# Kernel optimization log

Measured on AMD Instinct MI355X. Metric: run time of the kernel, lower is better.

## Reference

```python
import jax, jax.numpy as jnp
import numpy as np


def setup_inputs() -> dict:
    key = jax.random.key(0)
    ks = jax.random.split(key, 10)
    B, T, I, H = 64, 512, 512, 1024
    stdv = 1.0 / np.sqrt(H)
    u = lambda k, shape: jax.random.uniform(k, shape, jnp.float32, -stdv, stdv)
    return {
        "x": jax.random.normal(ks[0], (B, T, I), jnp.float32),
        "mask": jnp.ones((B, T, 1), jnp.float32),
        "s0": jnp.zeros((B, H), jnp.float32),
        "Ws": u(ks[1], (H, I)),
        "Wr": u(ks[2], (H, I)),
        "Wz": u(ks[3], (H, I)),
        "Us": u(ks[4], (H, H)),
        "Ur": u(ks[5], (H, H)),
        "Uz": u(ks[6], (H, H)),
        "bs": u(ks[7], (H,)),
        "br": u(ks[8], (H,)),
        "bz": u(ks[9], (H,)),
    }


def reference(x, mask, s0, Ws, Wr, Wz, Us, Ur, Uz, bs, br, bz):
    # Precompute input projections for all timesteps (batched GEMM).
    # x: [B,T,I]; xg: [B,T,H]
    xz = jnp.einsum("bti,hi->bth", x, Wz) + bz
    xr = jnp.einsum("bti,hi->bth", x, Wr) + br
    xs = jnp.einsum("bti,hi->bth", x, Ws) + bs

    def step(s, inp):
        xz_t, xr_t, xs_t, m_t = inp  # [B,H],[B,H],[B,H],[B,1]
        z = jax.nn.sigmoid(xz_t + s @ Uz.T)
        r = jax.nn.sigmoid(xr_t + s @ Ur.T)
        s_hat = jax.nn.relu(xs_t + (s * r) @ Us.T)
        s_new = (1.0 - z) * s + z * s_hat
        s_new = s * (1.0 - m_t) + s_new * m_t
        return s_new, s_new

    # scan over time: move T to leading axis
    xs_t = (jnp.swapaxes(xz, 0, 1), jnp.swapaxes(xr, 0, 1),
            jnp.swapaxes(xs, 0, 1), jnp.swapaxes(mask, 0, 1))
    _, ys = jax.lax.scan(step, s0, xs_t)  # ys: [T,B,H]
    return jnp.swapaxes(ys, 0, 1)  # [B,T,H]
```

## Files before the change

### kernel.cpp

```cpp
#include <hip/hip_runtime.h>

typedef unsigned short u16;
typedef unsigned long long u64;
typedef float f32x4 __attribute__((ext_vector_type(4)));
typedef short s16x8 __attribute__((ext_vector_type(8)));

#define B_ 64
#define T_ 512
#define I_ 512
#define H_ 1024
#define NBLK 256
#define NGRP 4
#define NMEM 64
#define NTHR 256

#define OFF_FLG 0
#define OFF_SBF 32768
#define OFF_RS  (OFF_SBF + 131072)
#define OFF_U   (OFF_RS + 131072)
#define OFF_W   (OFF_U + 6291456)

__device__ __forceinline__ u16 f2bf(float f) {
  unsigned u = __float_as_uint(f);
  return (u16)((u + 0x7FFFu + ((u >> 16) & 1u)) >> 16);
}

__device__ __forceinline__ s16x8 pack8(float4 a, float4 b) {
  s16x8 r;
  r[0] = (short)f2bf(a.x); r[1] = (short)f2bf(a.y);
  r[2] = (short)f2bf(a.z); r[3] = (short)f2bf(a.w);
  r[4] = (short)f2bf(b.x); r[5] = (short)f2bf(b.y);
  r[6] = (short)f2bf(b.z); r[7] = (short)f2bf(b.w);
  return r;
}

__device__ __forceinline__ void ld16_sc1(s16x8* d, const char* p) {
  asm volatile("global_load_dwordx4 %0, %1, off sc0 sc1" : "=v"(*d) : "v"(p));
}
__device__ __forceinline__ void st16_sc1(char* p, s16x8 v) {
  asm volatile("global_store_dwordx4 %0, %1, off sc0 sc1" :: "v"(p), "v"(v) : "memory");
}

__global__ void prep_kernel(const float* __restrict__ s0,
                            const float* __restrict__ Wz, const float* __restrict__ Wr,
                            const float* __restrict__ Ws, const float* __restrict__ Uz,
                            const float* __restrict__ Ur, const float* __restrict__ Us,
                            char* __restrict__ ws) {
  u16* ubf = (u16*)(ws + OFF_U);
  u16* wbf = (u16*)(ws + OFF_W);
  int tid = blockIdx.x * blockDim.x + threadIdx.x;
  int stride = gridDim.x * blockDim.x;
  const int NU = H_ * H_;
  for (int i = tid; i < NU; i += stride) {
    ubf[i] = f2bf(Uz[i]);
    ubf[NU + i] = f2bf(Ur[i]);
    ubf[2 * NU + i] = f2bf(Us[i]);
  }
  const int NW = H_ * I_;
  for (int i = tid; i < NW; i += stride) {
    wbf[i] = f2bf(Wz[i]);
    wbf[NW + i] = f2bf(Wr[i]);
    wbf[2 * NW + i] = f2bf(Ws[i]);
  }
  for (int f = tid; f < 4 * 32 * 64; f += stride) {
    int kc = (f >> 6) & 31, l = f & 63;
    int b = (f >> 11) * 16 + (l & 15);
    int k = kc * 32 + (l >> 4) * 8;
    const float* sp = s0 + (u64)b * H_ + k;
    ushort4 lo, hi;
    lo.x = f2bf(sp[0]); lo.y = f2bf(sp[1]); lo.z = f2bf(sp[2]); lo.w = f2bf(sp[3]);
    hi.x = f2bf(sp[4]); hi.y = f2bf(sp[5]); hi.z = f2bf(sp[6]); hi.w = f2bf(sp[7]);
    ushort4* dst = (ushort4*)(ws + OFF_SBF + (u64)f * 16);
    dst[0] = lo; dst[1] = hi;
  }
}

__device__ __forceinline__ void bar_poll(const unsigned* flags, int bg, unsigned bidx) {
  if (threadIdx.x < NMEM) {
    while (__hip_atomic_load(flags + (u64)(bg * NMEM + threadIdx.x) * 32,
                             __ATOMIC_RELAXED, __HIP_MEMORY_SCOPE_AGENT) < bidx)
      __builtin_amdgcn_s_sleep(1);
  }
  __syncthreads();
}

#define SWZ(row, byteInRow, rowShift) \
  (((((row) << (rowShift)) + (byteInRow))) ^ (((row) & 7) << 4))

__global__ __launch_bounds__(NTHR, 1) void scan_kernel(
    const float* __restrict__ x, const float* __restrict__ mask,
    const float* __restrict__ bz, const float* __restrict__ br,
    const float* __restrict__ bs, const float* __restrict__ s0,
    char* __restrict__ ws, float* __restrict__ out) {

  __shared__ u16 u_lds[3 * 16 * 1024];
  __shared__ u16 w_lds[3 * 16 * 512];
  __shared__ f32x4 red[4][2][64];
  __shared__ u16 tbf[16][16];
  __shared__ float tf32[16][16];

  char* fsb = ws + OFF_SBF;
  char* frb = ws + OFF_RS;
  const u16* ubf = (const u16*)(ws + OFF_U);
  const u16* wbf = (const u16*)(ws + OFF_W);
  unsigned* flags = (unsigned*)(ws + OFF_FLG);

  const int tid = threadIdx.x;
  const int jb = blockIdx.x;
  const int bg = jb & 3;
  const int hs = jb >> 2;
  const int h0 = hs * 16;
  const int lane = tid & 63;
  const int wave = tid >> 6;
  const int ln15 = lane & 15;
  const int kg = lane >> 4;
  const int h = h0 + ln15;

  for (int e = tid * 8; e < 3 * 16 * 1024; e += NTHR * 8) {
    int row = e >> 10, k = e & 1023;
    int g = row >> 4, hi = row & 15;
    uint4 v = *(const uint4*)(ubf + ((u64)(g * H_ + h0 + hi) * H_ + k));
    *(uint4*)((char*)u_lds + SWZ(row, (k << 1), 11)) = v;
  }
  for (int e = tid * 8; e < 3 * 16 * 512; e += NTHR * 8) {
    int row = e >> 9, k = e & 511;
    int g = row >> 4, hi = row & 15;
    uint4 v = *(const uint4*)(wbf + ((u64)(g * H_ + h0 + hi) * I_ + k));
    *(uint4*)((char*)w_lds + SWZ(row, (k << 1), 10)) = v;
  }
  const float bzv = bz[h];
  const float brv = br[h];
  const float bsv = bs[h];
  float sreg[4];
  #pragma unroll
  for (int j = 0; j < 4; ++j)
    sreg[j] = s0[(u64)(bg * 16 + kg * 4 + j) * H_ + h];
  __syncthreads();

  const char* sbase = fsb + (((u64)bg * 32 + wave * 8) * 64 + lane) * 16;
  const char* rbase = frb + (((u64)bg * 32 + wave * 8) * 64 + lane) * 16;
  char* sdst = fsb + (((u64)bg * 32 + (hs >> 1)) * 64 + lane + 32 * (hs & 1)) * 16;
  char* rdst = frb + (((u64)bg * 32 + (hs >> 1)) * 64 + lane + 32 * (hs & 1)) * 16;

  s16x8 xf[4];
  #pragma unroll
  for (int i = 0; i < 4; ++i) {
    const float* xp = x + ((u64)(bg * 16 + ln15) * T_) * I_ + (wave * 4 + i) * 32 + kg * 8;
    xf[i] = pack8(*(const float4*)xp, *(const float4*)(xp + 4));
  }
  f32x4 axz = {0.f,0.f,0.f,0.f}, axr = {0.f,0.f,0.f,0.f}, axs = {0.f,0.f,0.f,0.f};
  #pragma unroll
  for (int i = 0; i < 4; ++i) {
    const int cb = (wave * 4 + i) * 64 + kg * 16;
    s16x8 w0 = *(const s16x8*)((const char*)w_lds + SWZ(ln15, cb, 10));
    s16x8 w1 = *(const s16x8*)((const char*)w_lds + SWZ(16 + ln15, cb, 10));
    s16x8 w2 = *(const s16x8*)((const char*)w_lds + SWZ(32 + ln15, cb, 10));
    axz = __builtin_amdgcn_mfma_f32_16x16x32_bf16(xf[i], w0, axz, 0, 0, 0);
    axr = __builtin_amdgcn_mfma_f32_16x16x32_bf16(xf[i], w1, axr, 0, 0, 0);
    axs = __builtin_amdgcn_mfma_f32_16x16x32_bf16(xf[i], w2, axs, 0, 0, 0);
  }
  unsigned bidx = 0;

  for (int t = 0; t < T_; ++t) {
    float mv[4], zv[4];
    if (wave == 0) {
      #pragma unroll
      for (int j = 0; j < 4; ++j) mv[j] = mask[(u64)(bg * 16 + kg * 4 + j) * T_ + t];
    }

    s16x8 aS[8];
    #pragma unroll
    for (int q = 0; q < 8; ++q) ld16_sc1(&aS[q], sbase + q * 1024);
    __builtin_amdgcn_sched_barrier(0);
    asm volatile("s_waitcnt vmcnt(0)" ::: "memory");
    __builtin_amdgcn_sched_barrier(0);
    f32x4 accz = axz, accr = axr;
    #pragma unroll
    for (int q = 0; q < 8; ++q) {
      const int cb = (wave * 8 + q) * 64 + kg * 16;
      s16x8 b0 = *(const s16x8*)((const char*)u_lds + SWZ(ln15, cb, 11));
      s16x8 b1 = *(const s16x8*)((const char*)u_lds + SWZ(16 + ln15, cb, 11));
      accz = __builtin_amdgcn_mfma_f32_16x16x32_bf16(aS[q], b0, accz, 0, 0, 0);
      accr = __builtin_amdgcn_mfma_f32_16x16x32_bf16(aS[q], b1, accr, 0, 0, 0);
    }
    red[wave][0][lane] = accz;
    red[wave][1][lane] = accr;
    __syncthreads();
    ++bidx;
    if (wave == 0) {
      f32x4 az = red[0][0][lane], ar = red[0][1][lane];
      #pragma unroll
      for (int w = 1; w < 4; ++w) { az += red[w][0][lane]; ar += red[w][1][lane]; }
      #pragma unroll
      for (int j = 0; j < 4; ++j) {
        float z = 1.f / (1.f + __expf(-(az[j] + bzv)));
        float r = 1.f / (1.f + __expf(-(ar[j] + brv)));
        zv[j] = z;
        tbf[kg * 4 + j][ln15] = f2bf(sreg[j] * r);
      }
      if (lane < 32) {
        s16x8 v = *(const s16x8*)&tbf[lane & 15][(lane >> 4) * 8];
        st16_sc1(rdst, v);
      }
      asm volatile("s_waitcnt vmcnt(0)" ::: "memory");
      if (lane == 0)
        __hip_atomic_store(flags + (u64)(bg * NMEM + hs) * 32, bidx,
                           __ATOMIC_RELAXED, __HIP_MEMORY_SCOPE_AGENT);
    }
    bar_poll(flags, bg, bidx);

    s16x8 aR[8];
    #pragma unroll
    for (int q = 0; q < 8; ++q) ld16_sc1(&aR[q], rbase + q * 1024);
    __builtin_amdgcn_sched_barrier(0);
    asm volatile("s_waitcnt vmcnt(0)" ::: "memory");
    __builtin_amdgcn_sched_barrier(0);
    f32x4 accs = axs;
    #pragma unroll
    for (int q = 0; q < 8; ++q) {
      const int cb = (wave * 8 + q) * 64 + kg * 16;
      s16x8 b2 = *(const s16x8*)((const char*)u_lds + SWZ(32 + ln15, cb, 11));
      accs = __builtin_amdgcn_mfma_f32_16x16x32_bf16(aR[q], b2, accs, 0, 0, 0);
    }
    red[wave][0][lane] = accs;
    __syncthreads();
    ++bidx;
    if (wave == 0) {
      f32x4 as_ = red[0][0][lane];
      #pragma unroll
      for (int w = 1; w < 4; ++w) as_ += red[w][0][lane];
      #pragma unroll
      for (int j = 0; j < 4; ++j) {
        float shat = fmaxf(as_[j] + bsv, 0.f);
        float sn = (1.f - zv[j]) * sreg[j] + zv[j] * shat;
        float sf = sreg[j] + mv[j] * (sn - sreg[j]);
        sreg[j] = sf;
        tf32[kg * 4 + j][ln15] = sf;
        tbf[kg * 4 + j][ln15] = f2bf(sf);
      }
      if (lane < 32) {
        s16x8 v = *(const s16x8*)&tbf[lane & 15][(lane >> 4) * 8];
        st16_sc1(sdst, v);
      }
      asm volatile("s_waitcnt vmcnt(0)" ::: "memory");
      if (lane == 0)
        __hip_atomic_store(flags + (u64)(bg * NMEM + hs) * 32, bidx,
                           __ATOMIC_RELAXED, __HIP_MEMORY_SCOPE_AGENT);
      {
        f32x4 o = *(const f32x4*)&tf32[lane >> 2][(lane & 3) * 4];
        f32x4* op = (f32x4*)(out + ((u64)(bg * 16 + (lane >> 2)) * T_ + t) * H_ + h0 + (lane & 3) * 4);
        __builtin_nontemporal_store(o, op);
      }
    }
    if (t + 1 < T_) {
      #pragma unroll
      for (int i = 0; i < 4; ++i) {
        const float* xp = x + ((u64)(bg * 16 + ln15) * T_ + (t + 1)) * I_ + (wave * 4 + i) * 32 + kg * 8;
        xf[i] = pack8(*(const float4*)xp, *(const float4*)(xp + 4));
      }
      axz = f32x4{0.f,0.f,0.f,0.f}; axr = f32x4{0.f,0.f,0.f,0.f}; axs = f32x4{0.f,0.f,0.f,0.f};
      #pragma unroll
      for (int i = 0; i < 4; ++i) {
        const int cb = (wave * 4 + i) * 64 + kg * 16;
        s16x8 w0 = *(const s16x8*)((const char*)w_lds + SWZ(ln15, cb, 10));
        s16x8 w1 = *(const s16x8*)((const char*)w_lds + SWZ(16 + ln15, cb, 10));
        s16x8 w2 = *(const s16x8*)((const char*)w_lds + SWZ(32 + ln15, cb, 10));
        axz = __builtin_amdgcn_mfma_f32_16x16x32_bf16(xf[i], w0, axz, 0, 0, 0);
        axr = __builtin_amdgcn_mfma_f32_16x16x32_bf16(xf[i], w1, axr, 0, 0, 0);
        axs = __builtin_amdgcn_mfma_f32_16x16x32_bf16(xf[i], w2, axs, 0, 0, 0);
      }
    }
    bar_poll(flags, bg, bidx);
  }
}

extern "C" void kernel_launch(void* const* d_in, const int* in_sizes, int n_in,
                              void* d_out, int out_size, void* d_ws, size_t ws_size,
                              hipStream_t stream) {
  const float* x   = (const float*)d_in[0];
  const float* msk = (const float*)d_in[1];
  const float* s0  = (const float*)d_in[2];
  const float* Ws_ = (const float*)d_in[3];
  const float* Wr_ = (const float*)d_in[4];
  const float* Wz_ = (const float*)d_in[5];
  const float* Us_ = (const float*)d_in[6];
  const float* Ur_ = (const float*)d_in[7];
  const float* Uz_ = (const float*)d_in[8];
  const float* bs_ = (const float*)d_in[9];
  const float* br_ = (const float*)d_in[10];
  const float* bz_ = (const float*)d_in[11];
  float* out = (float*)d_out;
  char* ws = (char*)d_ws;

  (void)hipMemsetAsync(d_ws, 0, 32768, stream);
  hipLaunchKernelGGL(prep_kernel, dim3(1024), dim3(256), 0, stream,
                     s0, Wz_, Wr_, Ws_, Uz_, Ur_, Us_, ws);
  hipLaunchKernelGGL(scan_kernel, dim3(NBLK), dim3(NTHR), 0, stream,
                     x, msk, bz_, br_, bs_, s0, ws, out);
}
```

Baseline: 2.649 ms.

## Distribute gate epilogue across all waves with per-wave flags and polling

```diff
diff --git a/kernel.cpp b/kernel.cpp
--- a/kernel.cpp
+++ b/kernel.cpp
@@ -15,7 +15,7 @@
 #define NTHR 256
 
 #define OFF_FLG 0
-#define OFF_SBF 32768
+#define OFF_SBF 131072
 #define OFF_RS  (OFF_SBF + 131072)
 #define OFF_U   (OFF_RS + 131072)
 #define OFF_W   (OFF_U + 6291456)
@@ -75,15 +75,6 @@
   }
 }
 
-__device__ __forceinline__ void bar_poll(const unsigned* flags, int bg, unsigned bidx) {
-  if (threadIdx.x < NMEM) {
-    while (__hip_atomic_load(flags + (u64)(bg * NMEM + threadIdx.x) * 32,
-                             __ATOMIC_RELAXED, __HIP_MEMORY_SCOPE_AGENT) < bidx)
-      __builtin_amdgcn_s_sleep(1);
-  }
-  __syncthreads();
-}
-
 #define SWZ(row, byteInRow, rowShift) \
   (((((row) << (rowShift)) + (byteInRow))) ^ (((row) & 7) << 4))
 
@@ -95,9 +86,9 @@
 
   __shared__ u16 u_lds[3 * 16 * 1024];
   __shared__ u16 w_lds[3 * 16 * 512];
-  __shared__ f32x4 red[4][2][64];
-  __shared__ u16 tbf[16][16];
-  __shared__ float tf32[16][16];
+  __shared__ f32x4 red1[4][2][64];
+  __shared__ f32x4 red2[4][64];
+  __shared__ u16 tbw[4][4][16];
 
   char* fsb = ws + OFF_SBF;
   char* frb = ws + OFF_RS;
@@ -115,6 +106,7 @@
   const int ln15 = lane & 15;
   const int kg = lane >> 4;
   const int h = h0 + ln15;
+  const int Bl = 4 * wave + kg;
 
   for (int e = tid * 8; e < 3 * 16 * 1024; e += NTHR * 8) {
     int row = e >> 10, k = e & 1023;
@@ -131,16 +123,17 @@
   const float bzv = bz[h];
   const float brv = br[h];
   const float bsv = bs[h];
-  float sreg[4];
-  #pragma unroll
-  for (int j = 0; j < 4; ++j)
-    sreg[j] = s0[(u64)(bg * 16 + kg * 4 + j) * H_ + h];
+  float sreg = s0[(u64)(bg * 16 + Bl) * H_ + h];
+  float mv = mask[(u64)(bg * 16 + Bl) * T_];
   __syncthreads();
 
   const char* sbase = fsb + (((u64)bg * 32 + wave * 8) * 64 + lane) * 16;
   const char* rbase = frb + (((u64)bg * 32 + wave * 8) * 64 + lane) * 16;
-  char* sdst = fsb + (((u64)bg * 32 + (hs >> 1)) * 64 + lane + 32 * (hs & 1)) * 16;
-  char* rdst = frb + (((u64)bg * 32 + (hs >> 1)) * 64 + lane + 32 * (hs & 1)) * 16;
+  const int lp = (4 * wave + (lane & 3)) + 16 * ((hs & 1) * 2 + ((lane >> 2) & 1));
+  char* sdst = fsb + (((u64)bg * 32 + (hs >> 1)) * 64 + lp) * 16;
+  char* rdst = frb + (((u64)bg * 32 + (hs >> 1)) * 64 + lp) * 16;
+  unsigned* myflag = flags + ((u64)(bg * NMEM + hs) * 4 + wave) * 32;
+  const unsigned* pollp = flags + ((u64)(bg * NMEM + wave * 16 + ln15) * 4 + kg) * 32;
 
   s16x8 xf[4];
   #pragma unroll
@@ -160,14 +153,9 @@
     axs = __builtin_amdgcn_mfma_f32_16x16x32_bf16(xf[i], w2, axs, 0, 0, 0);
   }
   unsigned bidx = 0;
+  float zval = 0.f;
 
   for (int t = 0; t < T_; ++t) {
-    float mv[4], zv[4];
-    if (wave == 0) {
-      #pragma unroll
-      for (int j = 0; j < 4; ++j) mv[j] = mask[(u64)(bg * 16 + kg * 4 + j) * T_ + t];
-    }
-
     s16x8 aS[8];
     #pragma unroll
     for (int q = 0; q < 8; ++q) ld16_sc1(&aS[q], sbase + q * 1024);
@@ -183,31 +171,33 @@
       accz = __builtin_amdgcn_mfma_f32_16x16x32_bf16(aS[q], b0, accz, 0, 0, 0);
       accr = __builtin_amdgcn_mfma_f32_16x16x32_bf16(aS[q], b1, accr, 0, 0, 0);
     }
-    red[wave][0][lane] = accz;
-    red[wave][1][lane] = accr;
+    red1[wave][0][lane] = accz;
+    red1[wave][1][lane] = accr;
     __syncthreads();
     ++bidx;
-    if (wave == 0) {
-      f32x4 az = red[0][0][lane], ar = red[0][1][lane];
-      #pragma unroll
-      for (int w = 1; w < 4; ++w) { az += red[w][0][lane]; ar += red[w][1][lane]; }
-      #pragma unroll
-      for (int j = 0; j < 4; ++j) {
-        float z = 1.f / (1.f + __expf(-(az[j] + bzv)));
-        float r = 1.f / (1.f + __expf(-(ar[j] + brv)));
-        zv[j] = z;
-        tbf[kg * 4 + j][ln15] = f2bf(sreg[j] * r);
-      }
-      if (lane < 32) {
-        s16x8 v = *(const s16x8*)&tbf[lane & 15][(lane >> 4) * 8];
+    {
+      float az = 0.f, ar = 0.f;
+      #pragma unroll
+      for (int w2 = 0; w2 < 4; ++w2) {
+        const float* pz = (const float*)&red1[w2][0][wave * 16 + ln15];
+        const float* pr = (const float*)&red1[w2][1][wave * 16 + ln15];
+        az += pz[kg];
+        ar += pr[kg];
+      }
+      float z = 1.f / (1.f + __expf(-(az + bzv)));
+      float r = 1.f / (1.f + __expf(-(ar + brv)));
+      zval = z;
+      tbw[wave][kg][ln15] = f2bf(sreg * r);
+      if (lane < 8) {
+        s16x8 v = *(const s16x8*)&tbw[wave][lane & 3][((lane >> 2) & 1) * 8];
         st16_sc1(rdst, v);
       }
       asm volatile("s_waitcnt vmcnt(0)" ::: "memory");
       if (lane == 0)
-        __hip_atomic_store(flags + (u64)(bg * NMEM + hs) * 32, bidx,
-                           __ATOMIC_RELAXED, __HIP_MEMORY_SCOPE_AGENT);
-    }
-    bar_poll(flags, bg, bidx);
+        __hip_atomic_store(myflag, bidx, __ATOMIC_RELAXED, __HIP_MEMORY_SCOPE_AGENT);
+    }
+    while (__hip_atomic_load(pollp, __ATOMIC_RELAXED, __HIP_MEMORY_SCOPE_AGENT) < bidx)
+      __builtin_amdgcn_s_sleep(1);
 
     s16x8 aR[8];
     #pragma unroll
@@ -222,35 +212,29 @@
       s16x8 b2 = *(const s16x8*)((const char*)u_lds + SWZ(32 + ln15, cb, 11));
       accs = __builtin_amdgcn_mfma_f32_16x16x32_bf16(aR[q], b2, accs, 0, 0, 0);
     }
-    red[wave][0][lane] = accs;
+    red2[wave][lane] = accs;
     __syncthreads();
     ++bidx;
-    if (wave == 0) {
-      f32x4 as_ = red[0][0][lane];
-      #pragma unroll
-      for (int w = 1; w < 4; ++w) as_ += red[w][0][lane];
-      #pragma unroll
-      for (int j = 0; j < 4; ++j) {
-        float shat = fmaxf(as_[j] + bsv, 0.f);
-        float sn = (1.f - zv[j]) * sreg[j] + zv[j] * shat;
-        float sf = sreg[j] + mv[j] * (sn - sreg[j]);
-        sreg[j] = sf;
-        tf32[kg * 4 + j][ln15] = sf;
-        tbf[kg * 4 + j][ln15] = f2bf(sf);
-      }
-      if (lane < 32) {
-        s16x8 v = *(const s16x8*)&tbf[lane & 15][(lane >> 4) * 8];
+    {
+      float as_ = 0.f;
+      #pragma unroll
+      for (int w2 = 0; w2 < 4; ++w2) {
+        const float* ps = (const float*)&red2[w2][wave * 16 + ln15];
+        as_ += ps[kg];
+      }
+      float shat = fmaxf(as_ + bsv, 0.f);
+      float sn = (1.f - zval) * sreg + zval * shat;
+      float sf = sreg + mv * (sn - sreg);
+      sreg = sf;
+      tbw[wave][kg][ln15] = f2bf(sf);
+      if (lane < 8) {
+        s16x8 v = *(const s16x8*)&tbw[wave][lane & 3][((lane >> 2) & 1) * 8];
         st16_sc1(sdst, v);
       }
       asm volatile("s_waitcnt vmcnt(0)" ::: "memory");
       if (lane == 0)
-        __hip_atomic_store(flags + (u64)(bg * NMEM + hs) * 32, bidx,
-                           __ATOMIC_RELAXED, __HIP_MEMORY_SCOPE_AGENT);
-      {
-        f32x4 o = *(const f32x4*)&tf32[lane >> 2][(lane & 3) * 4];
-        f32x4* op = (f32x4*)(out + ((u64)(bg * 16 + (lane >> 2)) * T_ + t) * H_ + h0 + (lane & 3) * 4);
-        __builtin_nontemporal_store(o, op);
-      }
+        __hip_atomic_store(myflag, bidx, __ATOMIC_RELAXED, __HIP_MEMORY_SCOPE_AGENT);
+      __builtin_nontemporal_store(sf, out + ((u64)(bg * 16 + Bl) * T_ + t) * H_ + h);
     }
     if (t + 1 < T_) {
       #pragma unroll
@@ -269,8 +253,10 @@
         axr = __builtin_amdgcn_mfma_f32_16x16x32_bf16(xf[i], w1, axr, 0, 0, 0);
         axs = __builtin_amdgcn_mfma_f32_16x16x32_bf16(xf[i], w2, axs, 0, 0, 0);
       }
-    }
-    bar_poll(flags, bg, bidx);
+      mv = mask[(u64)(bg * 16 + Bl) * T_ + (t + 1)];
+    }
+    while (__hip_atomic_load(pollp, __ATOMIC_RELAXED, __HIP_MEMORY_SCOPE_AGENT) < bidx)
+      __builtin_amdgcn_s_sleep(1);
   }
 }
 
@@ -292,7 +278,7 @@
   float* out = (float*)d_out;
   char* ws = (char*)d_ws;
 
-  (void)hipMemsetAsync(d_ws, 0, 32768, stream);
+  (void)hipMemsetAsync(d_ws, 0, 131072, stream);
   hipLaunchKernelGGL(prep_kernel, dim3(1024), dim3(256), 0, stream,
                      s0, Wz_, Wr_, Ws_, Uz_, Ur_, Us_, ws);
   hipLaunchKernelGGL(scan_kernel, dim3(NBLK), dim3(NTHR), 0, stream,
```

New measurement: 3.175 ms. 1.2x slower.

## Replace flag barriers with per-slot sequence-tagged data and double-buffered parity

Applied to the files above, without the earlier changes.

```diff
diff --git a/kernel.cpp b/kernel.cpp
--- a/kernel.cpp
+++ b/kernel.cpp
@@ -4,20 +4,19 @@
 typedef unsigned long long u64;
 typedef float f32x4 __attribute__((ext_vector_type(4)));
 typedef short s16x8 __attribute__((ext_vector_type(8)));
+typedef int i32x4 __attribute__((ext_vector_type(4)));
 
 #define B_ 64
 #define T_ 512
 #define I_ 512
 #define H_ 1024
 #define NBLK 256
-#define NGRP 4
-#define NMEM 64
 #define NTHR 256
 
-#define OFF_FLG 0
-#define OFF_SBF 32768
-#define OFF_RS  (OFF_SBF + 131072)
-#define OFF_U   (OFF_RS + 131072)
+#define PAR_STRIDE 262144
+#define OFF_S   1024
+#define OFF_RS  (OFF_S + 2 * PAR_STRIDE)
+#define OFF_U   (OFF_RS + 2 * PAR_STRIDE)
 #define OFF_W   (OFF_U + 6291456)
 
 __device__ __forceinline__ u16 f2bf(float f) {
@@ -34,10 +33,10 @@
   return r;
 }
 
-__device__ __forceinline__ void ld16_sc1(s16x8* d, const char* p) {
+__device__ __forceinline__ void ld16v(i32x4* d, const char* p) {
   asm volatile("global_load_dwordx4 %0, %1, off sc0 sc1" : "=v"(*d) : "v"(p));
 }
-__device__ __forceinline__ void st16_sc1(char* p, s16x8 v) {
+__device__ __forceinline__ void st16v(char* p, i32x4 v) {
   asm volatile("global_store_dwordx4 %0, %1, off sc0 sc1" :: "v"(p), "v"(v) : "memory");
 }
 
@@ -62,26 +61,21 @@
     wbf[NW + i] = f2bf(Wr[i]);
     wbf[2 * NW + i] = f2bf(Ws[i]);
   }
-  for (int f = tid; f < 4 * 32 * 64; f += stride) {
-    int kc = (f >> 6) & 31, l = f & 63;
-    int b = (f >> 11) * 16 + (l & 15);
-    int k = kc * 32 + (l >> 4) * 8;
-    const float* sp = s0 + (u64)b * H_ + k;
-    ushort4 lo, hi;
-    lo.x = f2bf(sp[0]); lo.y = f2bf(sp[1]); lo.z = f2bf(sp[2]); lo.w = f2bf(sp[3]);
-    hi.x = f2bf(sp[4]); hi.y = f2bf(sp[5]); hi.z = f2bf(sp[6]); hi.w = f2bf(sp[7]);
-    ushort4* dst = (ushort4*)(ws + OFF_SBF + (u64)f * 16);
-    dst[0] = lo; dst[1] = hi;
-  }
-}
-
-__device__ __forceinline__ void bar_poll(const unsigned* flags, int bg, unsigned bidx) {
-  if (threadIdx.x < NMEM) {
-    while (__hip_atomic_load(flags + (u64)(bg * NMEM + threadIdx.x) * 32,
-                             __ATOMIC_RELAXED, __HIP_MEMORY_SCOPE_AGENT) < bidx)
-      __builtin_amdgcn_s_sleep(1);
-  }
-  __syncthreads();
+  char* sb = ws + OFF_S;
+  char* rb = ws + OFF_RS;
+  for (int i = tid; i < 4 * 16 * 256; i += stride) {
+    int bg = i >> 12, b = (i >> 8) & 15, kq = i & 255;
+    const float* sp = s0 + (u64)(bg * 16 + b) * H_ + kq * 4;
+    i32x4 u;
+    u.x = (int)f2bf(sp[0]) | ((int)f2bf(sp[1]) << 16);
+    u.y = (int)f2bf(sp[2]) | ((int)f2bf(sp[3]) << 16);
+    u.z = 0; u.w = 0;
+    *(i32x4*)(sb + (u64)i * 16) = u;
+    i32x4 z = {0, 0, -1, 0};
+    *(i32x4*)(sb + PAR_STRIDE + (u64)i * 16) = z;
+    *(i32x4*)(rb + (u64)i * 16) = z;
+    *(i32x4*)(rb + PAR_STRIDE + (u64)i * 16) = z;
+  }
 }
 
 #define SWZ(row, byteInRow, rowShift) \
@@ -95,15 +89,15 @@
 
   __shared__ u16 u_lds[3 * 16 * 1024];
   __shared__ u16 w_lds[3 * 16 * 512];
-  __shared__ f32x4 red[4][2][64];
+  __shared__ f32x4 red1[4][2][64];
+  __shared__ f32x4 red2[4][64];
   __shared__ u16 tbf[16][16];
   __shared__ float tf32[16][16];
 
-  char* fsb = ws + OFF_SBF;
-  char* frb = ws + OFF_RS;
+  char* sbuf = ws + OFF_S;
+  char* rbuf = ws + OFF_RS;
   const u16* ubf = (const u16*)(ws + OFF_U);
   const u16* wbf = (const u16*)(ws + OFF_W);
-  unsigned* flags = (unsigned*)(ws + OFF_FLG);
 
   const int tid = threadIdx.x;
   const int jb = blockIdx.x;
@@ -135,12 +129,13 @@
   #pragma unroll
   for (int j = 0; j < 4; ++j)
     sreg[j] = s0[(u64)(bg * 16 + kg * 4 + j) * H_ + h];
+  float mv[4];
+  #pragma unroll
+  for (int j = 0; j < 4; ++j) mv[j] = mask[(u64)(bg * 16 + kg * 4 + j) * T_];
   __syncthreads();
 
-  const char* sbase = fsb + (((u64)bg * 32 + wave * 8) * 64 + lane) * 16;
-  const char* rbase = frb + (((u64)bg * 32 + wave * 8) * 64 + lane) * 16;
-  char* sdst = fsb + (((u64)bg * 32 + (hs >> 1)) * 64 + lane + 32 * (hs & 1)) * 16;
-  char* rdst = frb + (((u64)bg * 32 + (hs >> 1)) * 64 + lane + 32 * (hs & 1)) * 16;
+  const u64 laneoff = (u64)(bg * 4096 + ln15 * 256 + wave * 64 + kg * 2) * 16;
+  const u64 prodoff = (u64)(bg * 4096 + (lane & 15) * 256 + hs * 4 + (lane >> 4)) * 16;
 
   s16x8 xf[4];
   #pragma unroll
@@ -159,38 +154,47 @@
     axr = __builtin_amdgcn_mfma_f32_16x16x32_bf16(xf[i], w1, axr, 0, 0, 0);
     axs = __builtin_amdgcn_mfma_f32_16x16x32_bf16(xf[i], w2, axs, 0, 0, 0);
   }
-  unsigned bidx = 0;
+  float zv[4];
 
   for (int t = 0; t < T_; ++t) {
-    float mv[4], zv[4];
-    if (wave == 0) {
-      #pragma unroll
-      for (int j = 0; j < 4; ++j) mv[j] = mask[(u64)(bg * 16 + kg * 4 + j) * T_ + t];
-    }
-
-    s16x8 aS[8];
-    #pragma unroll
-    for (int q = 0; q < 8; ++q) ld16_sc1(&aS[q], sbase + q * 1024);
-    __builtin_amdgcn_sched_barrier(0);
-    asm volatile("s_waitcnt vmcnt(0)" ::: "memory");
-    __builtin_amdgcn_sched_barrier(0);
+    const int par = t & 1;
+    i32x4 uu[16];
+    {
+      const char* sp1 = sbuf + (u64)par * PAR_STRIDE + laneoff;
+      for (;;) {
+        #pragma unroll
+        for (int q = 0; q < 8; ++q) {
+          ld16v(&uu[2 * q],     sp1 + q * 128);
+          ld16v(&uu[2 * q + 1], sp1 + q * 128 + 16);
+        }
+        asm volatile("s_waitcnt vmcnt(0)" ::: "memory");
+        __builtin_amdgcn_sched_barrier(0);
+        int ok = 1;
+        #pragma unroll
+        for (int i = 0; i < 16; ++i) ok &= (uu[i].z == t);
+        if (__all(ok)) break;
+        __builtin_amdgcn_s_sleep(1);
+      }
+    }
     f32x4 accz = axz, accr = axr;
     #pragma unroll
     for (int q = 0; q < 8; ++q) {
+      union { int w[4]; s16x8 v; } m;
+      m.w[0] = uu[2 * q].x; m.w[1] = uu[2 * q].y;
+      m.w[2] = uu[2 * q + 1].x; m.w[3] = uu[2 * q + 1].y;
       const int cb = (wave * 8 + q) * 64 + kg * 16;
       s16x8 b0 = *(const s16x8*)((const char*)u_lds + SWZ(ln15, cb, 11));
       s16x8 b1 = *(const s16x8*)((const char*)u_lds + SWZ(16 + ln15, cb, 11));
-      accz = __builtin_amdgcn_mfma_f32_16x16x32_bf16(aS[q], b0, accz, 0, 0, 0);
-      accr = __builtin_amdgcn_mfma_f32_16x16x32_bf16(aS[q], b1, accr, 0, 0, 0);
-    }
-    red[wave][0][lane] = accz;
-    red[wave][1][lane] = accr;
+      accz = __builtin_amdgcn_mfma_f32_16x16x32_bf16(m.v, b0, accz, 0, 0, 0);
+      accr = __builtin_amdgcn_mfma_f32_16x16x32_bf16(m.v, b1, accr, 0, 0, 0);
+    }
+    red1[wave][0][lane] = accz;
+    red1[wave][1][lane] = accr;
     __syncthreads();
-    ++bidx;
     if (wave == 0) {
-      f32x4 az = red[0][0][lane], ar = red[0][1][lane];
-      #pragma unroll
-      for (int w = 1; w < 4; ++w) { az += red[w][0][lane]; ar += red[w][1][lane]; }
+      f32x4 az = red1[0][0][lane], ar = red1[0][1][lane];
+      #pragma unroll
+      for (int w = 1; w < 4; ++w) { az += red1[w][0][lane]; ar += red1[w][1][lane]; }
       #pragma unroll
       for (int j = 0; j < 4; ++j) {
         float z = 1.f / (1.f + __expf(-(az[j] + bzv)));
@@ -198,37 +202,44 @@
         zv[j] = z;
         tbf[kg * 4 + j][ln15] = f2bf(sreg[j] * r);
       }
-      if (lane < 32) {
-        s16x8 v = *(const s16x8*)&tbf[lane & 15][(lane >> 4) * 8];
-        st16_sc1(rdst, v);
-      }
-      asm volatile("s_waitcnt vmcnt(0)" ::: "memory");
-      if (lane == 0)
-        __hip_atomic_store(flags + (u64)(bg * NMEM + hs) * 32, bidx,
-                           __ATOMIC_RELAXED, __HIP_MEMORY_SCOPE_AGENT);
-    }
-    bar_poll(flags, bg, bidx);
-
-    s16x8 aR[8];
-    #pragma unroll
-    for (int q = 0; q < 8; ++q) ld16_sc1(&aR[q], rbase + q * 1024);
-    __builtin_amdgcn_sched_barrier(0);
-    asm volatile("s_waitcnt vmcnt(0)" ::: "memory");
-    __builtin_amdgcn_sched_barrier(0);
+      uint2 d = *(const uint2*)&tbf[lane & 15][((lane >> 4)) * 4];
+      i32x4 pk; pk.x = (int)d.x; pk.y = (int)d.y; pk.z = t + 1; pk.w = 0;
+      st16v(rbuf + (u64)par * PAR_STRIDE + prodoff, pk);
+    }
+
+    {
+      const char* rp1 = rbuf + (u64)par * PAR_STRIDE + laneoff;
+      for (;;) {
+        #pragma unroll
+        for (int q = 0; q < 8; ++q) {
+          ld16v(&uu[2 * q],     rp1 + q * 128);
+          ld16v(&uu[2 * q + 1], rp1 + q * 128 + 16);
+        }
+        asm volatile("s_waitcnt vmcnt(0)" ::: "memory");
+        __builtin_amdgcn_sched_barrier(0);
+        int ok = 1;
+        #pragma unroll
+        for (int i = 0; i < 16; ++i) ok &= (uu[i].z == t + 1);
+        if (__all(ok)) break;
+        __builtin_amdgcn_s_sleep(1);
+      }
+    }
     f32x4 accs = axs;
     #pragma unroll
     for (int q = 0; q < 8; ++q) {
+      union { int w[4]; s16x8 v; } m;
+      m.w[0] = uu[2 * q].x; m.w[1] = uu[2 * q].y;
+      m.w[2] = uu[2 * q + 1].x; m.w[3] = uu[2 * q + 1].y;
       const int cb = (wave * 8 + q) * 64 + kg * 16;
       s16x8 b2 = *(const s16x8*)((const char*)u_lds + SWZ(32 + ln15, cb, 11));
-      accs = __builtin_amdgcn_mfma_f32_16x16x32_bf16(aR[q], b2, accs, 0, 0, 0);
-    }
-    red[wave][0][lane] = accs;
+      accs = __builtin_amdgcn_mfma_f32_16x16x32_bf16(m.v, b2, accs, 0, 0, 0);
+    }
+    red2[wave][lane] = accs;
     __syncthreads();
-    ++bidx;
     if (wave == 0) {
-      f32x4 as_ = red[0][0][lane];
-      #pragma unroll
-      for (int w = 1; w < 4; ++w) as_ += red[w][0][lane];
+      f32x4 as_ = red2[0][lane];
+      #pragma unroll
+      for (int w = 1; w < 4; ++w) as_ += red2[w][lane];
       #pragma unroll
       for (int j = 0; j < 4; ++j) {
         float shat = fmaxf(as_[j] + bsv, 0.f);
@@ -238,19 +249,12 @@
         tf32[kg * 4 + j][ln15] = sf;
         tbf[kg * 4 + j][ln15] = f2bf(sf);
       }
-      if (lane < 32) {
-        s16x8 v = *(const s16x8*)&tbf[lane & 15][(lane >> 4) * 8];
-        st16_sc1(sdst, v);
-      }
-      asm volatile("s_waitcnt vmcnt(0)" ::: "memory");
-      if (lane == 0)
-        __hip_atomic_store(flags + (u64)(bg * NMEM + hs) * 32, bidx,
-                           __ATOMIC_RELAXED, __HIP_MEMORY_SCOPE_AGENT);
-      {
-        f32x4 o = *(const f32x4*)&tf32[lane >> 2][(lane & 3) * 4];
-        f32x4* op = (f32x4*)(out + ((u64)(bg * 16 + (lane >> 2)) * T_ + t) * H_ + h0 + (lane & 3) * 4);
-        __builtin_nontemporal_store(o, op);
-      }
+      uint2 d = *(const uint2*)&tbf[lane & 15][((lane >> 4)) * 4];
+      i32x4 pk; pk.x = (int)d.x; pk.y = (int)d.y; pk.z = t + 1; pk.w = 0;
+      st16v(sbuf + (u64)((t + 1) & 1) * PAR_STRIDE + prodoff, pk);
+      f32x4 o = *(const f32x4*)&tf32[lane >> 2][(lane & 3) * 4];
+      f32x4* op = (f32x4*)(out + ((u64)(bg * 16 + (lane >> 2)) * T_ + t) * H_ + h0 + (lane & 3) * 4);
+      __builtin_nontemporal_store(o, op);
     }
     if (t + 1 < T_) {
       #pragma unroll
@@ -269,8 +273,11 @@
         axr = __builtin_amdgcn_mfma_f32_16x16x32_bf16(xf[i], w1, axr, 0, 0, 0);
         axs = __builtin_amdgcn_mfma_f32_16x16x32_bf16(xf[i], w2, axs, 0, 0, 0);
       }
-    }
-    bar_poll(flags, bg, bidx);
+      if (wave == 0) {
+        #pragma unroll
+        for (int j = 0; j < 4; ++j) mv[j] = mask[(u64)(bg * 16 + kg * 4 + j) * T_ + (t + 1)];
+      }
+    }
   }
 }
 
@@ -292,7 +299,6 @@
   float* out = (float*)d_out;
   char* ws = (char*)d_ws;
 
-  (void)hipMemsetAsync(d_ws, 0, 32768, stream);
   hipLaunchKernelGGL(prep_kernel, dim3(1024), dim3(256), 0, stream,
                      s0, Wz_, Wr_, Ws_, Uz_, Ur_, Us_, ws);
   hipLaunchKernelGGL(scan_kernel, dim3(NBLK), dim3(NTHR), 0, stream,
```

Measured after the change: 4.567 ms. 1.72x slower.
